# Kernel tuning notes

Measured on AMD Instinct MI355X. Metric: run time of the kernel, lower is better.

## Reference

```python
import jax, jax.numpy as jnp
import numpy as np

B, S, D, H, L, V = 8, 512, 1024, 16, 12, 30145
FF = 4 * D
NL = 2  # n_langs
EPS = 1e-12


def _ln(x, g, b):
    m = jnp.mean(x, axis=-1, keepdims=True)
    v = jnp.var(x, axis=-1, keepdims=True)
    return (x - m) * jax.lax.rsqrt(v + EPS) * g + b


def setup_inputs() -> dict:
    key = jax.random.key(0)
    ks = iter(jax.random.split(key, 32))
    std, estd = 0.02, 0.02
    d = {
        "input_ids": jax.random.randint(next(ks), (B, S), 0, V),
        "langs": jax.random.randint(next(ks), (B, S), 0, NL),
        "attention_mask": jnp.ones((B, S), jnp.float32),
        "word_emb": jax.random.normal(next(ks), (V, D), jnp.float32) * estd,
        "pos_emb": jax.random.normal(next(ks), (S, D), jnp.float32) * estd,
        "lang_emb": jax.random.normal(next(ks), (NL, D), jnp.float32) * estd,
        "ln_emb_g": jnp.ones((D,), jnp.float32),
        "ln_emb_b": jnp.zeros((D,), jnp.float32),
        "Wq": jax.random.normal(next(ks), (L, D, D), jnp.float32) * std,
        "bq": jnp.zeros((L, D), jnp.float32),
        "Wk": jax.random.normal(next(ks), (L, D, D), jnp.float32) * std,
        "bk": jnp.zeros((L, D), jnp.float32),
        "Wv": jax.random.normal(next(ks), (L, D, D), jnp.float32) * std,
        "bv": jnp.zeros((L, D), jnp.float32),
        "Wo": jax.random.normal(next(ks), (L, D, D), jnp.float32) * std,
        "bo": jnp.zeros((L, D), jnp.float32),
        "ln1_g": jnp.ones((L, D), jnp.float32),
        "ln1_b": jnp.zeros((L, D), jnp.float32),
        "W1": jax.random.normal(next(ks), (L, D, FF), jnp.float32) * std,
        "b1": jnp.zeros((L, FF), jnp.float32),
        "W2": jax.random.normal(next(ks), (L, FF, D), jnp.float32) * std,
        "b2": jnp.zeros((L, D), jnp.float32),
        "ln2_g": jnp.ones((L, D), jnp.float32),
        "ln2_b": jnp.zeros((L, D), jnp.float32),
    }
    return d


def reference(input_ids, langs, attention_mask, word_emb, pos_emb, lang_emb,
              ln_emb_g, ln_emb_b, Wq, bq, Wk, bk, Wv, bv, Wo, bo,
              ln1_g, ln1_b, W1, b1, W2, b2, ln2_g, ln2_b):
    dh = D // H
    scale = 1.0 / np.sqrt(dh).astype(np.float32)
    # embeddings: word + position + language, then LayerNorm, then pad-mask
    x = word_emb[input_ids] + pos_emb[None, :, :] + lang_emb[langs]  # [B,S,D]
    x = _ln(x, ln_emb_g, ln_emb_b)
    fmask = attention_mask  # [B,S], 1=keep
    x = x * fmask[:, :, None]
    neg = (-1e30) * (1.0 - fmask)[:, None, None, :]  # [B,1,1,S] additive mask

    def layer(x, p):
        Wq_, bq_, Wk_, bk_, Wv_, bv_, Wo_, bo_, g1, gb1, W1_, b1_, W2_, b2_, g2, gb2 = p
        q = ((x @ Wq_ + bq_) * scale).reshape(B, S, H, dh)
        k = (x @ Wk_ + bk_).reshape(B, S, H, dh)
        v = (x @ Wv_ + bv_).reshape(B, S, H, dh)
        scores = jnp.einsum('bqhd,bkhd->bhqk', q, k) + neg
        w = jax.nn.softmax(scores, axis=-1)
        ctx = jnp.einsum('bhqk,bkhd->bqhd', w, v).reshape(B, S, D)
        x = _ln(x + ctx @ Wo_ + bo_, g1, gb1)
        h = jax.nn.gelu(x @ W1_ + b1_, approximate=False)  # erf gelu as in source
        x = _ln(x + h @ W2_ + b2_, g2, gb2)
        x = x * fmask[:, :, None]
        return x, None

    params = (Wq, bq, Wk, bk, Wv, bv, Wo, bo, ln1_g, ln1_b, W1, b1, W2, b2, ln2_g, ln2_b)
    x, _ = jax.lax.scan(layer, x, params)
    return x
```

## Files before the change

kernel.cpp:

```cpp
#include <hip/hip_runtime.h>
#include <math.h>

typedef float  f32x4  __attribute__((ext_vector_type(4)));
typedef __bf16 bf16x8 __attribute__((ext_vector_type(8)));
typedef __bf16 bf16x4 __attribute__((ext_vector_type(4)));

#define DEV __device__ __forceinline__

DEV f32x4 mfma16(bf16x8 a, bf16x8 b, f32x4 c) {
    return __builtin_amdgcn_mfma_f32_16x16x32_bf16(a, b, c, 0, 0, 0);
}

DEV void async16(const void* g, void* l) {
    __builtin_amdgcn_global_load_lds((const __attribute__((address_space(1))) void*)g,
                                     (__attribute__((address_space(3))) void*)l, 16, 0, 0);
}

constexpr int B_  = 8;
constexpr int S_  = 512;
constexpr int D_  = 1024;
constexpr int H_  = 16;
constexpr int FF_ = 4096;
constexpr int ROWS = B_ * S_;

__global__ __launch_bounds__(256)
void embed_ln_kernel(const int* __restrict__ ids, const int* __restrict__ lgs,
                     const float* __restrict__ fmask,
                     const float* __restrict__ wemb, const float* __restrict__ pemb,
                     const float* __restrict__ lemb,
                     const float* __restrict__ g, const float* __restrict__ bb,
                     __bf16* __restrict__ xb)
{
    __shared__ float2 red[4];
    const int row = blockIdx.x;
    const int s   = row & (S_ - 1);
    const int t   = threadIdx.x;
    const int lane = t & 63, w = t >> 6;
    const int id = ids[row], lg = lgs[row];

    float4 wv = *(const float4*)(wemb + ((size_t)id << 10) + t * 4);
    float4 pv = *(const float4*)(pemb + ((size_t)s  << 10) + t * 4);
    float4 lv = *(const float4*)(lemb + ((size_t)lg << 10) + t * 4);
    float a[4] = { wv.x + pv.x + lv.x, wv.y + pv.y + lv.y,
                   wv.z + pv.z + lv.z, wv.w + pv.w + lv.w };

    float sm = a[0] + a[1] + a[2] + a[3];
    float sq = a[0]*a[0] + a[1]*a[1] + a[2]*a[2] + a[3]*a[3];
#pragma unroll
    for (int o = 32; o > 0; o >>= 1) { sm += __shfl_down(sm, o); sq += __shfl_down(sq, o); }
    if (lane == 0) red[w] = make_float2(sm, sq);
    __syncthreads();
    float ts = red[0].x + red[1].x + red[2].x + red[3].x;
    float tq = red[0].y + red[1].y + red[2].y + red[3].y;
    float mean = ts * (1.0f / D_);
    float var  = tq * (1.0f / D_) - mean * mean;
    float rs   = rsqrtf(var + 1e-12f);
    float fm   = fmask[row];

    float4 gv = *(const float4*)(g  + t * 4);
    float4 bv = *(const float4*)(bb + t * 4);
    bf16x4 ob;
    ob[0] = (__bf16)(((a[0]-mean)*rs*gv.x + bv.x) * fm);
    ob[1] = (__bf16)(((a[1]-mean)*rs*gv.y + bv.y) * fm);
    ob[2] = (__bf16)(((a[2]-mean)*rs*gv.z + bv.z) * fm);
    ob[3] = (__bf16)(((a[3]-mean)*rs*gv.w + bv.w) * fm);
    *(bf16x4*)(xb + ((size_t)row << 10) + t * 4) = ob;
}

template<int NP>
__global__ __launch_bounds__(256)
void ln_resN_kernel(const __bf16* __restrict__ xres, const __bf16* __restrict__ yp,
                    const float* __restrict__ g, const float* __restrict__ bb,
                    const float* __restrict__ fmask,
                    __bf16* __restrict__ xb_out, float* __restrict__ fout)
{
    constexpr size_t MN = (size_t)ROWS * D_;
    __shared__ float2 red[4];
    const int row = blockIdx.x;
    const int t   = threadIdx.x;
    const int lane = t & 63, w = t >> 6;
    const size_t base = ((size_t)row << 10) + t * 4;

    bf16x4 xv = *(const bf16x4*)(xres + base);
    float a[4] = { (float)xv[0], (float)xv[1], (float)xv[2], (float)xv[3] };
#pragma unroll
    for (int pslice = 0; pslice < NP; ++pslice) {
        bf16x4 yv = *(const bf16x4*)(yp + base + (size_t)pslice * MN);
#pragma unroll
        for (int j = 0; j < 4; ++j) a[j] += (float)yv[j];
    }

    float sm = a[0] + a[1] + a[2] + a[3];
    float sq = a[0]*a[0] + a[1]*a[1] + a[2]*a[2] + a[3]*a[3];
#pragma unroll
    for (int o = 32; o > 0; o >>= 1) { sm += __shfl_down(sm, o); sq += __shfl_down(sq, o); }
    if (lane == 0) red[w] = make_float2(sm, sq);
    __syncthreads();
    float ts = red[0].x + red[1].x + red[2].x + red[3].x;
    float tq = red[0].y + red[1].y + red[2].y + red[3].y;
    float mean = ts * (1.0f / D_);
    float var  = tq * (1.0f / D_) - mean * mean;
    float rs   = rsqrtf(var + 1e-12f);
    float fm   = fmask ? fmask[row] : 1.0f;

    float4 gv = *(const float4*)(g  + t * 4);
    float4 bv = *(const float4*)(bb + t * 4);
    float o0 = ((a[0]-mean)*rs*gv.x + bv.x) * fm;
    float o1 = ((a[1]-mean)*rs*gv.y + bv.y) * fm;
    float o2 = ((a[2]-mean)*rs*gv.z + bv.z) * fm;
    float o3 = ((a[3]-mean)*rs*gv.w + bv.w) * fm;
    bf16x4 ob; ob[0] = (__bf16)o0; ob[1] = (__bf16)o1; ob[2] = (__bf16)o2; ob[3] = (__bf16)o3;
    *(bf16x4*)(xb_out + base) = ob;
    if (fout) *(float4*)(fout + base) = make_float4(o0, o1, o2, o3);
}

__global__ __launch_bounds__(256)
void conv_all_kernel(const float* __restrict__ Wq, const float* __restrict__ Wk,
                     const float* __restrict__ Wv, const float* __restrict__ Wo,
                     const float* __restrict__ W1, const float* __restrict__ W2,
                     __bf16* __restrict__ qkvT, __bf16* __restrict__ woT,
                     __bf16* __restrict__ w1T, __bf16* __restrict__ w2T)
{
    __shared__ __bf16 tile[64][66];
    const int id = blockIdx.x;
    const int l  = id / 3072;
    int t = id - l * 3072;
    const size_t woff = (size_t)l * D_ * D_;
    const size_t foff = (size_t)l * D_ * FF_;
    const float* src; __bf16* dst; int K, N;
    if (t < 1024) {
        const int m = t >> 8; t &= 255; K = 1024; N = 1024;
        src = ((m == 0) ? Wq : (m == 1) ? Wk : (m == 2) ? Wv : Wo) + woff;
        dst = (m == 3) ? (woT + woff)
                       : (qkvT + (size_t)l * 3 * D_ * D_ + (size_t)m * D_ * D_);
    } else if (t < 2048) {
        t -= 1024; K = 1024; N = 4096; src = W1 + foff; dst = w1T + foff;
    } else {
        t -= 2048; K = 4096; N = 1024; src = W2 + foff; dst = w2T + foff;
    }
    const int ktiles = K >> 6;
    const int tk = t % ktiles, tn = t / ktiles;
    const int k0 = tk << 6, n0 = tn << 6;
    const int tt = threadIdx.x;
#pragma unroll
    for (int i = 0; i < 16; ++i) {
        int idx = i * 256 + tt;
        int r = idx >> 6, c = idx & 63;
        tile[c][r] = (__bf16)src[(size_t)(k0 + r) * N + n0 + c];
    }
    __syncthreads();
#pragma unroll
    for (int i = 0; i < 16; ++i) {
        int idx = i * 256 + tt;
        int r = idx >> 6, c = idx & 63;
        dst[(size_t)(n0 + r) * K + k0 + c] = tile[r][c];
    }
}

template<int EPI>
__global__ __launch_bounds__(512, 2)
void gemm256_kernel(const __bf16* __restrict__ A, const __bf16* __restrict__ Bt,
                    const float* __restrict__ b0, const float* __restrict__ b1,
                    const float* __restrict__ b2,
                    __bf16* __restrict__ o0, __bf16* __restrict__ o1,
                    __bf16* __restrict__ o2, __bf16* __restrict__ oP,
                    int M, int N, int K, int Kloc, int nTn, int tiles)
{
    __shared__ __bf16 lds[65536];
    const int tid  = threadIdx.x;
    const int lane = tid & 63;
    const int w    = tid >> 6;
    const int wr   = w >> 2, wc = w & 3;

    const int nwg = gridDim.x, bid = blockIdx.x;
    const int cpx = nwg >> 3;
    const int bswz = (bid & 7) * cpx + (bid >> 3);
    const int slice = bswz / tiles;
    const int tile  = bswz % tiles;
    const int bm = tile / nTn, bn = tile % nTn;
    const int m0 = bm << 8, n0 = bn << 8;
    const int ks = slice * Kloc;

    const int rrT = tid >> 3;
    const size_t swzK  = (size_t)(((tid & 7) ^ (rrT & 7)) * 8);
    const size_t aoff0 = (size_t)rrT * K + swzK;
    const size_t boff0 = (size_t)((rrT >> 5) * 64 + (rrT & 31)) * K + swzK;
    const size_t boff1 = (size_t)(((rrT >> 5) + 2) * 64 + (rrT & 31)) * K + swzK;
    const int wub = w * 512;

    const int aread = (wr * 64 + (lane & 15)) * 64;
    const int bread = (wc * 32 + (lane & 15)) * 64;
    const int csw0 = ((      (lane >> 4) * 16) ^ ((lane & 7) << 4)) >> 1;
    const int csw1 = ((64 +  (lane >> 4) * 16) ^ ((lane & 7) << 4)) >> 1;

    f32x4 acc[8][4] = {};
    bf16x8 a_[4][2], b_[2][2];

#define ST_A(p,h,kt) do {                                                     \
    const size_t gb = (size_t)(m0 + (h) * 64) * K + (kt);                     \
    async16(A + gb + aoff0,                  lds + ((p)*2+(h))*8192 + wub);   \
    async16(A + gb + (size_t)128*K + aoff0,  lds + ((p)*2+(h))*8192 + 4096 + wub); \
} while (0)
#define ST_B(p,h,kt) do {                                                     \
    const size_t gb = (size_t)(n0 + (h) * 32) * K + (kt);                     \
    async16(Bt + gb + boff0, lds + 32768 + ((p)*2+(h))*8192 + wub);           \
    async16(Bt + gb + boff1, lds + 32768 + ((p)*2+(h))*8192 + 4096 + wub);    \
} while (0)
#define DS_A(p,h) do {                                                        \
    const __bf16* base_ = lds + ((p)*2+(h))*8192 + aread;                     \
    _Pragma("unroll") for (int m_ = 0; m_ < 4; ++m_) {                        \
        a_[m_][0] = *(const bf16x8*)(base_ + m_*1024 + csw0);                 \
        a_[m_][1] = *(const bf16x8*)(base_ + m_*1024 + csw1);                 \
    }                                                                         \
} while (0)
#define DS_B(p,h) do {                                                        \
    const __bf16* base_ = lds + 32768 + ((p)*2+(h))*8192 + bread;             \
    _Pragma("unroll") for (int n_ = 0; n_ < 2; ++n_) {                        \
        b_[n_][0] = *(const bf16x8*)(base_ + n_*1024 + csw0);                 \
        b_[n_][1] = *(const bf16x8*)(base_ + n_*1024 + csw1);                 \
    }                                                                         \
} while (0)
#define MM(mb,nb) do {                                                        \
    _Pragma("unroll") for (int m_ = 0; m_ < 4; ++m_)                          \
    _Pragma("unroll") for (int n_ = 0; n_ < 2; ++n_)                          \
    _Pragma("unroll") for (int k_ = 0; k_ < 2; ++k_)                          \
        acc[(mb)+m_][(nb)+n_] = mfma16(a_[m_][k_], b_[n_][k_], acc[(mb)+m_][(nb)+n_]); \
} while (0)
#define SYNC do { __builtin_amdgcn_s_barrier();                               \
    asm volatile("s_waitcnt lgkmcnt(0)" ::: "memory");                        \
    __builtin_amdgcn_s_setprio(1); } while (0)
#define PEND do { __builtin_amdgcn_s_setprio(0);                              \
    __builtin_amdgcn_s_barrier(); } while (0)

    ST_A(0,0, ks);      ST_B(0,1, ks);      ST_A(0,1, ks);      ST_B(0,0, ks);
    ST_A(1,0, ks + 64); ST_B(1,1, ks + 64); ST_A(1,1, ks + 64);
    asm volatile("s_waitcnt vmcnt(6)" ::: "memory");
    __builtin_amdgcn_s_barrier();

    const int nIter = Kloc >> 7;
    for (int i = 0; i < nIter; ++i) {
        const bool nl = (i != nIter - 1);
        const int kt1 = ks + (2*i+1) * 64;
        const int kt2 = ks + (2*i+2) * 64;
        const int kt3 = kt2 + 64;
        DS_A(0,0); DS_B(0,0); ST_B(1,0,kt1);
        SYNC; MM(0,0); PEND;
        DS_B(0,1); if (nl) ST_A(0,0,kt2);
        SYNC; MM(0,2); PEND;
        DS_A(0,1); if (nl) ST_B(0,1,kt2);
        SYNC; MM(4,2); PEND;
        DS_B(0,0); if (nl) ST_A(0,1,kt2);
        SYNC; MM(4,0);
        __builtin_amdgcn_s_setprio(0);
        if (nl) asm volatile("s_waitcnt vmcnt(6)" ::: "memory");
        else    asm volatile("s_waitcnt vmcnt(0)" ::: "memory");
        __builtin_amdgcn_s_barrier();
        DS_A(1,0); DS_B(1,0); if (nl) ST_B(0,0,kt2);
        SYNC; MM(0,0); PEND;
        DS_B(1,1); if (nl) ST_A(1,0,kt3);
        SYNC; MM(0,2); PEND;
        DS_A(1,1); if (nl) ST_B(1,1,kt3);
        SYNC; MM(4,2); PEND;
        DS_B(1,0); if (nl) ST_A(1,1,kt3);
        SYNC; MM(4,0);
        __builtin_amdgcn_s_setprio(0);
        if (nl) asm volatile("s_waitcnt vmcnt(6)" ::: "memory");
        __builtin_amdgcn_s_barrier();
    }
#undef ST_A
#undef ST_B
#undef DS_A
#undef DS_B
#undef MM
#undef SYNC
#undef PEND

    const int mrow = m0 + wr * 128 + (lane >> 4) * 4;
    const int ncol = n0 + wc * 64 + (lane & 15);
    if (EPI == 0) {
        const int sel = n0 >> 10;
        const int nc = ncol & 1023;
        if (sel < 2) {
            __bf16* out = (sel == 0) ? o0 : o1;
            const float* bp = (sel == 0) ? b0 : b1;
            const float scl = (sel == 0) ? 0.125f : 1.0f;
#pragma unroll
            for (int ni = 0; ni < 4; ++ni) {
                const float bvv = bp[nc + ni * 16];
#pragma unroll
                for (int mi = 0; mi < 8; ++mi)
#pragma unroll
                    for (int r = 0; r < 4; ++r)
                        out[(size_t)(mrow + mi * 16 + r) * D_ + nc + ni * 16] =
                            (__bf16)((acc[mi][ni][r] + bvv) * scl);
            }
        } else {
#pragma unroll
            for (int ni = 0; ni < 4; ++ni) {
                const int dhf = nc + ni * 16;
                const float bvv = b2[dhf];
                const int hh = dhf >> 6, dh = dhf & 63;
#pragma unroll
                for (int mi = 0; mi < 8; ++mi) {
                    const int gm0 = mrow + mi * 16;
                    const int bb_ = gm0 >> 9, s0 = gm0 & 511;
                    bf16x4 pk;
#pragma unroll
                    for (int r = 0; r < 4; ++r) pk[r] = (__bf16)(acc[mi][ni][r] + bvv);
                    *(bf16x4*)(o2 + ((size_t)((bb_ * 16 + hh) * 64 + dh) << 9) + s0) = pk;
                }
            }
        }
    } else if (EPI == 2) {
#pragma unroll
        for (int ni = 0; ni < 4; ++ni) {
            const float bvv = b0[ncol + ni * 16];
#pragma unroll
            for (int mi = 0; mi < 8; ++mi)
#pragma unroll
                for (int r = 0; r < 4; ++r) {
                    float v = acc[mi][ni][r] + bvv;
                    float ge = 0.5f * v * (1.0f + erff(v * 0.70710678118654752f));
                    o0[(size_t)(mrow + mi * 16 + r) * N + ncol + ni * 16] = (__bf16)ge;
                }
        }
    } else {
        __bf16* Y = oP + (size_t)slice * M * N;
#pragma unroll
        for (int ni = 0; ni < 4; ++ni) {
            const float bvv = (slice == 0) ? b0[ncol + ni * 16] : 0.0f;
#pragma unroll
            for (int mi = 0; mi < 8; ++mi)
#pragma unroll
                for (int r = 0; r < 4; ++r)
                    Y[(size_t)(mrow + mi * 16 + r) * N + ncol + ni * 16] =
                        (__bf16)(acc[mi][ni][r] + bvv);
        }
    }
}

__global__ __launch_bounds__(256, 2)
void attn_kernel(const __bf16* __restrict__ q, const __bf16* __restrict__ k,
                 const __bf16* __restrict__ vT, const float* __restrict__ fmask,
                 __bf16* __restrict__ ctx)
{
    __shared__ __bf16 Ks[256 * 64];
    __shared__ __bf16 Vt[64 * 256];
    __shared__ float  negm[S_];
    const int bid = blockIdx.x;
    const int qt = bid & 7, h = (bid >> 3) & 15, b = bid >> 7;
    const int tid = threadIdx.x, lane = tid & 63, w = tid >> 6;
    const int g = lane >> 4, q15 = lane & 15, r7 = lane & 7;

    const __bf16* kbase  = k  + ((size_t)b * S_) * D_ + h * 64;
    const __bf16* vTbase = vT + ((size_t)((b * 16 + h) * 64) << 9);
    char* kl = (char*)Ks + (tid & ~63) * 16;
    char* vl = (char*)Vt + (tid & ~63) * 16;
    const int srow  = tid >> 3;
    const int sslot = (tid & 7) ^ (srow & 7);
    const int vrow  = tid >> 5;
#define ST_K(c) do { _Pragma("unroll") for (int i_ = 0; i_ < 8; ++i_) {       \
        const int s_ = (c) * 256 + i_ * 32 + srow;                            \
        async16(kbase + (size_t)s_ * D_ + sslot * 8, kl + i_ * 4096); } } while (0)
#define ST_V(c) do { _Pragma("unroll") for (int i_ = 0; i_ < 8; ++i_) {       \
        const int d_ = i_ * 8 + vrow;                                         \
        async16(vTbase + ((size_t)d_ << 9) + (c) * 256 +                      \
                (((tid & 31) ^ (d_ & 7)) << 3), vl + i_ * 4096); } } while (0)

    ST_K(0);
    for (int i = tid; i < S_; i += 256) negm[i] = (fmask[b * S_ + i] - 1.0f) * 1e30f;

    const __bf16* qbase = q + ((size_t)b * S_ + qt * 64 + w * 16) * D_ + h * 64;
    const bf16x8 qf0 = *(const bf16x8*)(qbase + (size_t)q15 * D_ + g * 8);
    const bf16x8 qf1 = *(const bf16x8*)(qbase + (size_t)q15 * D_ + 32 + g * 8);

    f32x4 sc[32];
#pragma unroll
    for (int i = 0; i < 32; ++i) { sc[i][0] = 0.f; sc[i][1] = 0.f; sc[i][2] = 0.f; sc[i][3] = 0.f; }

#define QKT(c) do { _Pragma("unroll") for (int nf = 0; nf < 16; ++nf) {       \
        const __bf16* kr = Ks + (nf * 16 + q15) * 64;                         \
        const bf16x8 kf0 = *(const bf16x8*)(kr + ((g ^ r7) << 3));            \
        const bf16x8 kf1 = *(const bf16x8*)(kr + (((g + 4) ^ r7) << 3));      \
        sc[(c)*16+nf] = mfma16(kf0, qf0, sc[(c)*16+nf]);                      \
        sc[(c)*16+nf] = mfma16(kf1, qf1, sc[(c)*16+nf]); } } while (0)

    __syncthreads();
    ST_V(0);
    QKT(0);
    __syncthreads();
    ST_K(1);
    __syncthreads();
    QKT(1);

    float mx = -3e38f;
#pragma unroll
    for (int i = 0; i < 32; ++i) {
        const float4 nm4 = *(const float4*)(negm + ((i >> 4) * 256 + (i & 15) * 16 + 4 * g));
        sc[i][0] += nm4.x; sc[i][1] += nm4.y; sc[i][2] += nm4.z; sc[i][3] += nm4.w;
        mx = fmaxf(mx, fmaxf(fmaxf(sc[i][0], sc[i][1]), fmaxf(sc[i][2], sc[i][3])));
    }
    mx = fmaxf(mx, __shfl_xor(mx, 16));
    mx = fmaxf(mx, __shfl_xor(mx, 32));
    float sum = 0.f;
#pragma unroll
    for (int i = 0; i < 32; ++i)
#pragma unroll
        for (int r = 0; r < 4; ++r) { float pp = __expf(sc[i][r] - mx); sc[i][r] = pp; sum += pp; }
    sum += __shfl_xor(sum, 16);
    sum += __shfl_xor(sum, 32);
    const float inv = 1.0f / sum;

    __bf16* P = Ks + w * 4096;
    f32x4 co[4] = {};
#define WR_P(c) do { _Pragma("unroll") for (int i_ = 0; i_ < 16; ++i_) {      \
        bf16x4 pk;                                                            \
        _Pragma("unroll") for (int r = 0; r < 4; ++r) pk[r] = (__bf16)sc[(c)*16+i_][r]; \
        *(bf16x4*)(P + q15 * 256 + ((i_ * 16 + 4 * g) ^ (8 * r7))) = pk; } } while (0)
#define PV() do { _Pragma("unroll") for (int kt = 0; kt < 8; ++kt) {          \
        const bf16x8 pf = *(const bf16x8*)(P + q15 * 256 + ((kt * 32 + 8 * g) ^ (8 * r7))); \
        _Pragma("unroll") for (int nf = 0; nf < 4; ++nf) {                    \
            const int d_ = nf * 16 + q15;                                     \
            const bf16x8 vf = *(const bf16x8*)(Vt + d_ * 256 + ((kt * 32 + 8 * g) ^ (8 * r7))); \
            co[nf] = mfma16(vf, pf, co[nf]); } } } while (0)

    __syncthreads();
    WR_P(0);
    __syncthreads();
    PV();
    __syncthreads();
    WR_P(1);
    ST_V(1);
    __syncthreads();
    PV();
#undef ST_K
#undef ST_V
#undef QKT
#undef WR_P
#undef PV

    __bf16* cb = ctx + ((size_t)b * S_ + qt * 64 + w * 16 + q15) * D_ + h * 64;
#pragma unroll
    for (int nf = 0; nf < 4; ++nf) {
        bf16x4 o4;
#pragma unroll
        for (int r = 0; r < 4; ++r) o4[r] = (__bf16)(co[nf][r] * inv);
        *(bf16x4*)(cb + nf * 16 + 4 * g) = o4;
    }
}

extern "C" void kernel_launch(void* const* d_in, const int* in_sizes, int n_in,
                              void* d_out, int out_size, void* d_ws, size_t ws_size,
                              hipStream_t stream)
{
    (void)in_sizes; (void)n_in; (void)out_size; (void)ws_size;
    const int*   ids   = (const int*)d_in[0];
    const int*   lgs   = (const int*)d_in[1];
    const float* amask = (const float*)d_in[2];
    const float* wemb  = (const float*)d_in[3];
    const float* pemb  = (const float*)d_in[4];
    const float* lemb  = (const float*)d_in[5];
    const float* lng   = (const float*)d_in[6];
    const float* lnbv  = (const float*)d_in[7];
    const float* Wq = (const float*)d_in[8];  const float* bq = (const float*)d_in[9];
    const float* Wk = (const float*)d_in[10]; const float* bk = (const float*)d_in[11];
    const float* Wv = (const float*)d_in[12]; const float* bv = (const float*)d_in[13];
    const float* Wo = (const float*)d_in[14]; const float* bo = (const float*)d_in[15];
    const float* g1 = (const float*)d_in[16]; const float* be1 = (const float*)d_in[17];
    const float* W1 = (const float*)d_in[18]; const float* b1 = (const float*)d_in[19];
    const float* W2 = (const float*)d_in[20]; const float* b2 = (const float*)d_in[21];
    const float* g2 = (const float*)d_in[22]; const float* be2 = (const float*)d_in[23];

    char* p = (char*)d_ws;
    auto take = [&](size_t n) { char* r = p; p += (n + 255) & ~(size_t)255; return r; };
    __bf16* xb    = (__bf16*)take((size_t)ROWS * D_ * 2);
    __bf16* qb    = (__bf16*)take((size_t)ROWS * D_ * 2);
    __bf16* kb    = (__bf16*)take((size_t)ROWS * D_ * 2);
    __bf16* vT    = (__bf16*)take((size_t)ROWS * D_ * 2);
    __bf16* cxb   = (__bf16*)take((size_t)ROWS * D_ * 2);
    __bf16* hb    = (__bf16*)take((size_t)ROWS * FF_ * 2);
    __bf16* ybp   = (__bf16*)take((size_t)4 * ROWS * D_ * 2);
    __bf16* wqkvT = (__bf16*)take((size_t)12 * 3 * D_ * D_ * 2);
    __bf16* woT   = (__bf16*)take((size_t)12 * D_ * D_ * 2);
    __bf16* w1T   = (__bf16*)take((size_t)12 * D_ * FF_ * 2);
    __bf16* w2T   = (__bf16*)take((size_t)12 * FF_ * D_ * 2);

    const int gQKV = (ROWS / 256) * (3 * D_ / 256);
    const int gF1  = (ROWS / 256) * (FF_ / 256);
    const int gF2  = 4 * (ROWS / 256) * (D_ / 256);
    const int gWo  = 4 * (ROWS / 256) * (D_ / 256);

    conv_all_kernel<<<12 * 3072, 256, 0, stream>>>(Wq, Wk, Wv, Wo, W1, W2,
                                                   wqkvT, woT, w1T, w2T);

    embed_ln_kernel<<<ROWS, 256, 0, stream>>>(ids, lgs, amask, wemb, pemb, lemb, lng, lnbv, xb);

    for (int l = 0; l < 12; ++l) {
        __bf16* wqkvL = wqkvT + (size_t)l * 3 * D_ * D_;
        __bf16* woL   = woT   + (size_t)l * D_ * D_;
        __bf16* w1L   = w1T   + (size_t)l * D_ * FF_;
        __bf16* w2L   = w2T   + (size_t)l * FF_ * D_;

        gemm256_kernel<0><<<gQKV, 512, 0, stream>>>(xb, wqkvL, bq + l * D_, bk + l * D_, bv + l * D_,
                                                    qb, kb, vT, nullptr,
                                                    ROWS, 3 * D_, D_, D_, 12, gQKV);

        attn_kernel<<<B_ * H_ * (S_ / 64), 256, 0, stream>>>(qb, kb, vT, amask, cxb);

        gemm256_kernel<3><<<gWo, 512, 0, stream>>>(cxb, woL, bo + l * D_, nullptr, nullptr,
                                                   nullptr, nullptr, nullptr, ybp,
                                                   ROWS, D_, D_, D_ / 4, 4, 64);
        ln_resN_kernel<4><<<ROWS, 256, 0, stream>>>(xb, ybp, g1 + l * D_, be1 + l * D_,
                                                    nullptr, xb, nullptr);

        gemm256_kernel<2><<<gF1, 512, 0, stream>>>(xb, w1L, b1 + l * FF_, nullptr, nullptr,
                                                   hb, nullptr, nullptr, nullptr,
                                                   ROWS, FF_, D_, D_, 16, gF1);
        gemm256_kernel<3><<<gF2, 512, 0, stream>>>(hb, w2L, b2 + l * D_, nullptr, nullptr,
                                                   nullptr, nullptr, nullptr, ybp,
                                                   ROWS, D_, FF_, D_, 4, 64);

        float* dst = (l == 11) ? (float*)d_out : nullptr;
        ln_resN_kernel<4><<<ROWS, 256, 0, stream>>>(xb, ybp, g2 + l * D_, be2 + l * D_,
                                                    amask, xb, dst);
    }
}
```

Measured before the change: 2.587 ms.

## Vectorize weight transpose and load full K/V per 128-row attention block

The weight conversion kernel now reads float4 from global memory and writes bf16x8 vectors through a swizzled LDS tile, replacing scalar 4-byte loads and 2-byte stores. This targets the memory-bound fp32-to-bf16 transpose of all layer weights. The attention kernel moves to 512-thread blocks that each cover 128 query rows and stage the whole 512-key K and V^T in LDS at once. That halves the K/V reloads per head but drops the staged load/compute overlap, raises LDS use and limits the kernel to one block per CU.

```diff
diff --git a/kernel.cpp b/kernel.cpp
--- a/kernel.cpp
+++ b/kernel.cpp
@@ -121,7 +121,7 @@
                      __bf16* __restrict__ qkvT, __bf16* __restrict__ woT,
                      __bf16* __restrict__ w1T, __bf16* __restrict__ w2T)
 {
-    __shared__ __bf16 tile[64][66];
+    __shared__ __bf16 tile[64 * 72];
     const int id = blockIdx.x;
     const int l  = id / 3072;
     int t = id - l * 3072;
@@ -142,18 +142,27 @@
     const int tk = t % ktiles, tn = t / ktiles;
     const int k0 = tk << 6, n0 = tn << 6;
     const int tt = threadIdx.x;
-#pragma unroll
-    for (int i = 0; i < 16; ++i) {
-        int idx = i * 256 + tt;
-        int r = idx >> 6, c = idx & 63;
-        tile[c][r] = (__bf16)src[(size_t)(k0 + r) * N + n0 + c];
-    }
-    __syncthreads();
-#pragma unroll
-    for (int i = 0; i < 16; ++i) {
-        int idx = i * 256 + tt;
-        int r = idx >> 6, c = idx & 63;
-        dst[(size_t)(n0 + r) * K + k0 + c] = tile[r][c];
+
+    const int kr = tt >> 4;
+    const int tc = (tt & 15) * 4;
+#pragma unroll
+    for (int i = 0; i < 4; ++i) {
+        const int k = i * 16 + kr;
+        float4 v = *(const float4*)(src + (size_t)(k0 + k) * N + n0 + tc);
+        const int sl = k >> 3, kb = k & 7;
+        tile[(tc    ) * 72 + ((sl ^ ((tc    ) & 7)) << 3) + kb] = (__bf16)v.x;
+        tile[(tc + 1) * 72 + ((sl ^ ((tc + 1) & 7)) << 3) + kb] = (__bf16)v.y;
+        tile[(tc + 2) * 72 + ((sl ^ ((tc + 2) & 7)) << 3) + kb] = (__bf16)v.z;
+        tile[(tc + 3) * 72 + ((sl ^ ((tc + 3) & 7)) << 3) + kb] = (__bf16)v.w;
+    }
+    __syncthreads();
+    const int nr = tt >> 3;
+    const int kc = tt & 7;
+#pragma unroll
+    for (int pp = 0; pp < 2; ++pp) {
+        const int n = pp * 32 + nr;
+        bf16x8 vv = *(const bf16x8*)(tile + n * 72 + ((kc ^ (n & 7)) << 3));
+        *(bf16x8*)(dst + (size_t)(n0 + n) * K + k0 + kc * 8) = vv;
     }
 }
 
@@ -339,16 +348,16 @@
     }
 }
 
-__global__ __launch_bounds__(256, 2)
+__global__ __launch_bounds__(512, 1)
 void attn_kernel(const __bf16* __restrict__ q, const __bf16* __restrict__ k,
                  const __bf16* __restrict__ vT, const float* __restrict__ fmask,
                  __bf16* __restrict__ ctx)
 {
-    __shared__ __bf16 Ks[256 * 64];
-    __shared__ __bf16 Vt[64 * 256];
+    __shared__ __bf16 Ks[512 * 64];
+    __shared__ __bf16 Vt[64 * 512];
     __shared__ float  negm[S_];
     const int bid = blockIdx.x;
-    const int qt = bid & 7, h = (bid >> 3) & 15, b = bid >> 7;
+    const int qt = bid & 3, h = (bid >> 2) & 15, b = bid >> 6;
     const int tid = threadIdx.x, lane = tid & 63, w = tid >> 6;
     const int g = lane >> 4, q15 = lane & 15, r7 = lane & 7;
 
@@ -358,19 +367,20 @@
     char* vl = (char*)Vt + (tid & ~63) * 16;
     const int srow  = tid >> 3;
     const int sslot = (tid & 7) ^ (srow & 7);
-    const int vrow  = tid >> 5;
-#define ST_K(c) do { _Pragma("unroll") for (int i_ = 0; i_ < 8; ++i_) {       \
-        const int s_ = (c) * 256 + i_ * 32 + srow;                            \
-        async16(kbase + (size_t)s_ * D_ + sslot * 8, kl + i_ * 4096); } } while (0)
-#define ST_V(c) do { _Pragma("unroll") for (int i_ = 0; i_ < 8; ++i_) {       \
-        const int d_ = i_ * 8 + vrow;                                         \
-        async16(vTbase + ((size_t)d_ << 9) + (c) * 256 +                      \
-                (((tid & 31) ^ (d_ & 7)) << 3), vl + i_ * 4096); } } while (0)
-
-    ST_K(0);
-    for (int i = tid; i < S_; i += 256) negm[i] = (fmask[b * S_ + i] - 1.0f) * 1e30f;
-
-    const __bf16* qbase = q + ((size_t)b * S_ + qt * 64 + w * 16) * D_ + h * 64;
+
+#pragma unroll
+    for (int i = 0; i < 8; ++i) {
+        const int s = i * 64 + srow;
+        async16(kbase + (size_t)s * D_ + sslot * 8, kl + i * 8192);
+    }
+#pragma unroll
+    for (int i = 0; i < 8; ++i) {
+        const int d = i * 8 + w;
+        async16(vTbase + ((size_t)d << 9) + (((tid & 63) ^ (d & 7)) << 3), vl + i * 8192);
+    }
+    if (tid < S_) negm[tid] = (fmask[b * S_ + tid] - 1.0f) * 1e30f;
+
+    const __bf16* qbase = q + ((size_t)b * S_ + qt * 128 + w * 16) * D_ + h * 64;
     const bf16x8 qf0 = *(const bf16x8*)(qbase + (size_t)q15 * D_ + g * 8);
     const bf16x8 qf1 = *(const bf16x8*)(qbase + (size_t)q15 * D_ + 32 + g * 8);
 
@@ -378,25 +388,20 @@
 #pragma unroll
     for (int i = 0; i < 32; ++i) { sc[i][0] = 0.f; sc[i][1] = 0.f; sc[i][2] = 0.f; sc[i][3] = 0.f; }
 
-#define QKT(c) do { _Pragma("unroll") for (int nf = 0; nf < 16; ++nf) {       \
-        const __bf16* kr = Ks + (nf * 16 + q15) * 64;                         \
-        const bf16x8 kf0 = *(const bf16x8*)(kr + ((g ^ r7) << 3));            \
-        const bf16x8 kf1 = *(const bf16x8*)(kr + (((g + 4) ^ r7) << 3));      \
-        sc[(c)*16+nf] = mfma16(kf0, qf0, sc[(c)*16+nf]);                      \
-        sc[(c)*16+nf] = mfma16(kf1, qf1, sc[(c)*16+nf]); } } while (0)
-
-    __syncthreads();
-    ST_V(0);
-    QKT(0);
-    __syncthreads();
-    ST_K(1);
-    __syncthreads();
-    QKT(1);
+    __syncthreads();
+#pragma unroll
+    for (int nf = 0; nf < 32; ++nf) {
+        const __bf16* kr = Ks + (nf * 16 + q15) * 64;
+        const bf16x8 kf0 = *(const bf16x8*)(kr + ((g ^ r7) << 3));
+        const bf16x8 kf1 = *(const bf16x8*)(kr + (((g + 4) ^ r7) << 3));
+        sc[nf] = mfma16(kf0, qf0, sc[nf]);
+        sc[nf] = mfma16(kf1, qf1, sc[nf]);
+    }
 
     float mx = -3e38f;
 #pragma unroll
     for (int i = 0; i < 32; ++i) {
-        const float4 nm4 = *(const float4*)(negm + ((i >> 4) * 256 + (i & 15) * 16 + 4 * g));
+        const float4 nm4 = *(const float4*)(negm + i * 16 + 4 * g);
         sc[i][0] += nm4.x; sc[i][1] += nm4.y; sc[i][2] += nm4.z; sc[i][3] += nm4.w;
         mx = fmaxf(mx, fmaxf(fmaxf(sc[i][0], sc[i][1]), fmaxf(sc[i][2], sc[i][3])));
     }
@@ -417,29 +422,26 @@
         bf16x4 pk;                                                            \
         _Pragma("unroll") for (int r = 0; r < 4; ++r) pk[r] = (__bf16)sc[(c)*16+i_][r]; \
         *(bf16x4*)(P + q15 * 256 + ((i_ * 16 + 4 * g) ^ (8 * r7))) = pk; } } while (0)
-#define PV() do { _Pragma("unroll") for (int kt = 0; kt < 8; ++kt) {          \
+#define PV(c) do { _Pragma("unroll") for (int kt = 0; kt < 8; ++kt) {         \
         const bf16x8 pf = *(const bf16x8*)(P + q15 * 256 + ((kt * 32 + 8 * g) ^ (8 * r7))); \
         _Pragma("unroll") for (int nf = 0; nf < 4; ++nf) {                    \
             const int d_ = nf * 16 + q15;                                     \
-            const bf16x8 vf = *(const bf16x8*)(Vt + d_ * 256 + ((kt * 32 + 8 * g) ^ (8 * r7))); \
+            const bf16x8 vf = *(const bf16x8*)(Vt + d_ * 512 +                \
+                (((c) * 256 + kt * 32 + 8 * g) ^ (8 * r7)));                  \
             co[nf] = mfma16(vf, pf, co[nf]); } } } while (0)
 
     __syncthreads();
     WR_P(0);
     __syncthreads();
-    PV();
+    PV(0);
     __syncthreads();
     WR_P(1);
-    ST_V(1);
-    __syncthreads();
-    PV();
-#undef ST_K
-#undef ST_V
-#undef QKT
+    __syncthreads();
+    PV(1);
 #undef WR_P
 #undef PV
 
-    __bf16* cb = ctx + ((size_t)b * S_ + qt * 64 + w * 16 + q15) * D_ + h * 64;
+    __bf16* cb = ctx + ((size_t)b * S_ + qt * 128 + w * 16 + q15) * D_ + h * 64;
 #pragma unroll
     for (int nf = 0; nf < 4; ++nf) {
         bf16x4 o4;
@@ -505,7 +507,7 @@
                                                     qb, kb, vT, nullptr,
                                                     ROWS, 3 * D_, D_, D_, 12, gQKV);
 
-        attn_kernel<<<B_ * H_ * (S_ / 64), 256, 0, stream>>>(qb, kb, vT, amask, cxb);
+        attn_kernel<<<B_ * H_ * (S_ / 128), 512, 0, stream>>>(qb, kb, vT, amask, cxb);
 
         gemm256_kernel<3><<<gWo, 512, 0, stream>>>(cxb, woL, bo + l * D_, nullptr, nullptr,
                                                    nullptr, nullptr, nullptr, ybp,
```

Result: no change. 2.578 ms (-0.3%).
